# Kernel optimization log

Measured on AMD Instinct MI355X. Metric: run time of the kernel, lower is better.

The kernel has to match this reference:

```python
import jax, jax.numpy as jnp
import numpy as np

CHN = 64
C8 = CHN // 8          # 8
ANG_IN = 5
ANG_OUT = 5
BU, V, H, W = 8, ANG_IN, 64, 64


def setup_inputs() -> dict:
    key = jax.random.key(0)
    ks = jax.random.split(key, 7)
    s = 0.05
    buffer = jax.random.normal(ks[0], (BU, CHN, V, H, W), jnp.float32)
    # 1x1x1 Conv3d weights stored as [out_ch, in_ch]
    Wq = jax.random.normal(ks[1], (C8, CHN), jnp.float32) * s
    Wk = jax.random.normal(ks[2], (C8, CHN), jnp.float32) * s
    Wv = jax.random.normal(ks[3], (C8 * ANG_OUT, CHN), jnp.float32) * s
    Wc = jax.random.normal(ks[4], (C8 * ANG_OUT, CHN), jnp.float32) * s
    # out block: Conv3d(40->64, k=(1,1,7), pad (0,0,3)); Conv3d(64->64, k=(7,1,1), pad (3,0,0))
    W1 = jax.random.normal(ks[5], (CHN, C8 * ANG_IN, 1, 1, 7), jnp.float32) * s
    W2 = jax.random.normal(ks[6], (CHN, CHN, 7, 1, 1), jnp.float32) * s
    return {"buffer": buffer, "Wq": Wq, "Wk": Wk, "Wv": Wv, "Wc": Wc, "W1": W1, "W2": W2}


def _pointwise(Wo, x):
    # 1x1x1 Conv3d == channel GEMM
    return jnp.einsum('oc,bcvhw->bovhw', Wo, x)


def reference(buffer, Wq, Wk, Wv, Wc, W1, W2):
    bu, c, v, h, w = buffer.shape
    q = _pointwise(Wq, buffer)      # [bu, c8, v, h, w]
    k = _pointwise(Wk, buffer)      # [bu, c8, v, h, w]
    val = _pointwise(Wv, buffer)    # [bu, c8*ar_out, v, h, w]

    def flat(x):  # 'bu c v h w -> bu c h (v w)'
        return x.transpose(0, 1, 3, 2, 4).reshape(bu, x.shape[1], h, v * w)

    qf, kf, vf = flat(q), flat(k), flat(val)
    attn = jax.nn.softmax(jnp.einsum('bchm,bchn->bhmn', qf, kf), axis=-1)  # [bu,h,vw,vw]
    out = jnp.einsum('bhmn,bchn->bchm', attn, vf)                          # [bu,c8*ar_out,h,vw]
    out = out.reshape(bu, -1, h, v, w).transpose(0, 1, 3, 2, 4)            # [bu,c8*ar_out,v,h,w]

    out = out + _pointwise(Wc, buffer)
    # 'bu (c ar_out) v h w -> bu (c v) ar_out h w'
    c8 = out.shape[1] // ANG_OUT
    out = out.reshape(bu, c8, ANG_OUT, v, h, w).transpose(0, 1, 3, 2, 4, 5)
    out = out.reshape(bu, c8 * v, ANG_OUT, h, w)

    dn = ('NCDHW', 'OIDHW', 'NCDHW')
    out = jax.nn.relu(jax.lax.conv_general_dilated(
        out, W1, (1, 1, 1), [(0, 0), (0, 0), (3, 3)], dimension_numbers=dn))
    out = jax.nn.relu(jax.lax.conv_general_dilated(
        out, W2, (1, 1, 1), [(3, 3), (0, 0), (0, 0)], dimension_numbers=dn))
    return out  # [bu, chn, ar_out, h, w]
```

## Files before the change

### kernel.cpp

```cpp
#include <hip/hip_runtime.h>
#include <math.h>


typedef __attribute__((ext_vector_type(8))) short bf16x8;
typedef __attribute__((ext_vector_type(4))) short bf16x4;
typedef __attribute__((ext_vector_type(4))) float fp32x4;
typedef __attribute__((ext_vector_type(8))) unsigned short u16x8;

#define OFF_WPJ_US  0
#define OFF_W1P_US  12288
#define OFF_W2P_US  30720
#define OFF_QFH_US  13166592
#define OFF_KFH_US  14477312
#define OFF_VTH_US  15788032
#define OFF_ZB16_US 23652352
#define OFF_Z       29696

__device__ inline unsigned short f2b(float f) {
    unsigned u = __builtin_bit_cast(unsigned, f);
    u = (u + 0x7fffu + ((u >> 16) & 1u)) >> 16;
    return (unsigned short)u;
}

#if __has_builtin(__builtin_amdgcn_mfma_f32_16x16x16bf16_1k)
#define MFMA16(a, b, c) __builtin_amdgcn_mfma_f32_16x16x16bf16_1k(a, b, c, 0, 0, 0)
#else
static __device__ inline fp32x4 mfma16_asm(bf16x4 a, bf16x4 b, fp32x4 c) {
    asm("v_mfma_f32_16x16x16_bf16 %0, %1, %2, %0" : "+v"(c) : "v"(a), "v"(b));
    return c;
}
#define MFMA16(a, b, c) mfma16_asm(a, b, c)
#endif

__global__ void prep_weights(const float* __restrict__ Wq, const float* __restrict__ Wk,
                             const float* __restrict__ Wv, const float* __restrict__ Wc,
                             const float* __restrict__ W1, const float* __restrict__ W2,
                             float* __restrict__ ws) {
    int e = blockIdx.x * 256 + threadIdx.x;
    unsigned short* us = (unsigned short*)ws;
    if (e < 6144) {
        int mt = e >> 10, kt = (e >> 9) & 1, lane = (e >> 3) & 63, j = e & 7;
        int m = mt * 16 + (lane & 15);
        int k = kt * 32 + ((lane >> 4) & 3) * 8 + j;
        float v;
        if (m < 8)       v = Wq[m * 64 + k];
        else if (m < 16) v = Wk[(m - 8) * 64 + k];
        else if (m < 56) v = Wv[(m - 16) * 64 + k];
        else             v = Wc[(m - 56) * 64 + k];
        us[OFF_WPJ_US + e] = f2b(v);
    } else if (e < 6144 + 18432) {
        int t = e - 6144;
        int j = t & 7, lane = (t >> 3) & 63, ks = (t >> 9) % 9, wid = t / 4608;
        int oc = wid * 16 + (lane & 15);
        int k = ks * 32 + (lane >> 4) * 8 + j;
        float v = 0.f;
        if (k < 280) { int kw = k / 40, ic = k % 40; v = W1[oc * 280 + ic * 7 + kw]; }
        us[OFF_W1P_US + t] = f2b(v);
    } else if (e < 6144 + 18432 + 28672) {
        int t = e - 6144 - 18432;
        int j = t & 7, lane = (t >> 3) & 63, kk = (t >> 9) & 1, kd = (t >> 10) % 7, wid = t / 7168;
        int oc = wid * 16 + (lane & 15);
        int ic = kk * 32 + (lane >> 4) * 8 + j;
        us[OFF_W2P_US + t] = f2b(W2[oc * 448 + ic * 7 + kd]);
    }
}

__global__ __launch_bounds__(256) void proj_kernel(const float* __restrict__ buf,
                                                   float* __restrict__ ws) {
    __shared__ alignas(16) float xs[64 * 64];
    int b = blockIdx.x;
    int h = b & 63;
    int v = (b >> 6) % 5;
    int bu = b / 320;
    int tid = threadIdx.x, wid = tid >> 6, lane = tid & 63;
    int col = lane & 15, quad = lane >> 4;

    const float* xbase = buf + ((bu * 64) * 5 + v) * 4096 + h * 64;
    for (int e = tid; e < 1024; e += 256) {
        int c = e >> 4, wq = e & 15;
        *(float4*)&xs[c * 64 + wq * 4] = *(const float4*)&xbase[c * 20480 + wq * 4];
    }

    const unsigned short* wpj = (const unsigned short*)ws + OFF_WPJ_US;
    bf16x8 aw[6][2];
    #pragma unroll
    for (int mt = 0; mt < 6; mt++)
        #pragma unroll
        for (int kt = 0; kt < 2; kt++)
            aw[mt][kt] = *(const bf16x8*)&wpj[((mt * 2 + kt) * 64 + lane) * 8];

    __syncthreads();

    int n0 = wid * 16;
    bf16x8 xb[2];
    #pragma unroll
    for (int kt = 0; kt < 2; kt++) {
        u16x8 t;
        #pragma unroll
        for (int j = 0; j < 8; j++)
            t[j] = f2b(xs[(kt * 32 + quad * 8 + j) * 64 + n0 + col]);
        xb[kt] = __builtin_bit_cast(bf16x8, t);
    }

    fp32x4 acc[6];
    #pragma unroll
    for (int mt = 0; mt < 6; mt++) acc[mt] = (fp32x4){0.f, 0.f, 0.f, 0.f};
    #pragma unroll
    for (int kt = 0; kt < 2; kt++)
        #pragma unroll
        for (int mt = 0; mt < 6; mt++)
            acc[mt] = __builtin_amdgcn_mfma_f32_16x16x32_bf16(aw[mt][kt], xb[kt], acc[mt], 0, 0, 0);

    int site = bu * 64 + h;
    int w = n0 + col;
    int n_flat = v * 64 + w;
    unsigned short* base = (unsigned short*)ws;
    unsigned short* qfh = base + OFF_QFH_US;
    unsigned short* kfh = base + OFF_KFH_US;
    unsigned short* vth = base + OFF_VTH_US;
    float* z = ws + OFF_Z;

    {
        ushort4 o;
        o.x = f2b(acc[0][0]); o.y = f2b(acc[0][1]); o.z = f2b(acc[0][2]); o.w = f2b(acc[0][3]);
        if (quad < 2) *(ushort4*)&qfh[(site * 320 + n_flat) * 8 + quad * 4] = o;
        else          *(ushort4*)&kfh[(site * 320 + n_flat) * 8 + (quad - 2) * 4] = o;
    }
    #pragma unroll
    for (int r = 0; r < 4; r++) {
        vth[(site * 48 + quad * 4 + r) * 320 + n_flat]      = f2b(acc[1][r]);
        vth[(site * 48 + 16 + quad * 4 + r) * 320 + n_flat] = f2b(acc[2][r]);
    }
    if (quad < 2) {
        #pragma unroll
        for (int r = 0; r < 4; r++)
            vth[(site * 48 + 32 + quad * 4 + r) * 320 + n_flat] = f2b(acc[3][r]);
    } else {
        #pragma unroll
        for (int r = 0; r < 4; r++) {
            int jc = (quad - 2) * 4 + r;
            z[((bu * 40 + (jc / 5) * 5 + v) * 5 + (jc % 5)) * 4096 + h * 64 + w] = acc[3][r];
        }
    }
    #pragma unroll
    for (int r = 0; r < 4; r++) {
        int jc4 = 8 + quad * 4 + r;
        z[((bu * 40 + (jc4 / 5) * 5 + v) * 5 + (jc4 % 5)) * 4096 + h * 64 + w] = acc[4][r];
        int jc5 = 24 + quad * 4 + r;
        z[((bu * 40 + (jc5 / 5) * 5 + v) * 5 + (jc5 % 5)) * 4096 + h * 64 + w] = acc[5][r];
    }
    if (wid == 3) {
        #pragma unroll
        for (int j = 40; j < 48; j++)
            vth[(site * 48 + j) * 320 + v * 64 + lane] =
                (j == 40) ? (unsigned short)0x3F80 : (unsigned short)0;
    }
}

__global__ __launch_bounds__(256, 2) void attn_kernel(float* __restrict__ ws) {
    __shared__ alignas(16) short vt[48 * 328];
    __shared__ alignas(16) short kl[320 * 8];

    int bid = blockIdx.x;
    int chunk = bid >> 9;
    int site = bid & 511;
    int bu = site >> 6, h = site & 63;
    int tid = threadIdx.x;
    int wid = tid >> 6, lane = tid & 63;
    int col = lane & 15, quad = lane >> 4;

    const unsigned short* base = (const unsigned short*)ws;
    const unsigned short* qfh = base + OFF_QFH_US + site * 320 * 8;
    const unsigned short* kfh = base + OFF_KFH_US + site * 320 * 8;
    const unsigned short* vsrc = base + OFF_VTH_US + site * 48 * 320;
    float* z = ws + OFF_Z;
    unsigned short* zb16 = (unsigned short*)ws + OFF_ZB16_US;

    for (int e = tid; e < 48 * 40; e += 256) {
        int row = e / 40, c8o = e % 40;
        *(u16x8*)&vt[row * 328 + c8o * 8] = *(const u16x8*)&vsrc[row * 320 + c8o * 8];
    }
    for (int e = tid; e < 320; e += 256)
        *(u16x8*)&kl[e * 8] = *(const u16x8*)&kfh[e * 8];
    __syncthreads();

    int off0[4], off1[4], off2[4];
    #pragma unroll
    for (int r = 0; r < 4; r++) {
        int j0 = quad * 4 + r, j1 = j0 + 16, j2 = j0 + 32;
        off0[r] = ((j0 / 5) * 25 + j0 % 5) * 4096;
        off1[r] = ((j1 / 5) * 25 + j1 % 5) * 4096;
        off2[r] = ((j2 / 5) * 25 + j2 % 5) * 4096;
    }

    int mt = chunk * 4 + wid;
    int m0 = mt * 16;

    int v_idx = m0 >> 6, w0 = m0 & 63;
    int sbase = (bu * 200 + v_idx * 5) * 4096 + h * 64 + w0 + col;
    float* zb = z + sbase;
    float zold0[4], zold1[4], zold2[4];
    #pragma unroll
    for (int r = 0; r < 4; r++) {
        zold0[r] = zb[off0[r]];
        zold1[r] = zb[off1[r]];
        zold2[r] = (quad < 2) ? zb[off2[r]] : 0.f;
    }

    bf16x8 qa = (bf16x8)0;
    if (quad == 0) qa = *(const bf16x8*)&qfh[(m0 + col) * 8];

    fp32x4 acc0 = {0.f, 0.f, 0.f, 0.f}, acc1 = acc0, acc2 = acc0;

    for (int cc = 0; cc < 4; cc++) {
        fp32x4 sT[5];
        #pragma unroll
        for (int u = 0; u < 5; u++) {
            int nt = cc * 5 + u;
            bf16x8 kb = *(const bf16x8*)&kl[(nt * 16 + col) * 8];
            sT[u] = __builtin_amdgcn_mfma_f32_16x16x32_bf16(
                kb, qa, (fp32x4){0.f, 0.f, 0.f, 0.f}, 0, 0, 0);
        }
        #pragma unroll
        for (int u = 0; u < 5; u++) {
            int nt = cc * 5 + u;
            bf16x4 pa;
            #pragma unroll
            for (int r = 0; r < 4; r++) pa[r] = (short)f2b(__expf(sT[u][r]));
            const short* vb = &vt[nt * 16 + quad * 4];
            acc0 = MFMA16(*(const bf16x4*)&vb[(col) * 328],      pa, acc0);
            acc1 = MFMA16(*(const bf16x4*)&vb[(16 + col) * 328], pa, acc1);
            acc2 = MFMA16(*(const bf16x4*)&vb[(32 + col) * 328], pa, acc2);
        }
    }

    float L = __shfl(acc2[0], 32 + col, 64);
    float inv = 1.f / L;

    unsigned short* zsb = zb16 + sbase;
    #pragma unroll
    for (int r = 0; r < 4; r++) {
        zsb[off0[r]] = f2b(zold0[r] + acc0[r] * inv);
        zsb[off1[r]] = f2b(zold1[r] + acc1[r] * inv);
        if (quad < 2) zsb[off2[r]] = f2b(zold2[r] + acc2[r] * inv);
    }
}

__global__ __launch_bounds__(256) void conv12_mfma(float* __restrict__ ws,
                                                   float* __restrict__ out) {
    __shared__ alignas(16) unsigned short ol[320 * 72];
    __shared__ alignas(16) unsigned short zl2[2][72 * 40];
    int b = blockIdx.x;
    int bu = b >> 6, h = b & 63;
    int tid = threadIdx.x, wid = tid >> 6, lane = tid & 63;
    int col = lane & 15, quad = lane >> 4;
    const unsigned short* zb16 = (const unsigned short*)ws + OFF_ZB16_US;

    const unsigned short* w1p = (const unsigned short*)ws + OFF_W1P_US;
    bf16x8 a1[9];
    #pragma unroll
    for (int ks = 0; ks < 9; ks++)
        a1[ks] = *(const bf16x8*)&w1p[((wid * 9 + ks) * 64 + lane) * 8];

    #define STAGE_AR(ar_, bufi_)                                                          \
        {                                                                                 \
            unsigned short* zb_ = zl2[bufi_];                                             \
            if (tid < 160) {                                                              \
                int wpi = tid / 20, icd = tid % 20;                                       \
                int wp = wpi < 3 ? wpi : wpi + 64;                                        \
                ((unsigned*)zb_)[wp * 20 + icd] = 0u;                                     \
            }                                                                             \
            for (int icq = wid; icq < 10; icq += 4) {                                     \
                const unsigned short* src = zb16 + ((bu * 40 + icq * 4) * 5 + (ar_)) * 4096 + h * 64 + lane; \
                ushort4 v4;                                                               \
                v4.x = src[0];                                                            \
                v4.y = src[20480];                                                        \
                v4.z = src[40960];                                                        \
                v4.w = src[61440];                                                        \
                *(ushort4*)&zb_[(3 + lane) * 40 + icq * 4] = v4;                          \
            }                                                                             \
        }

    STAGE_AR(0, 0);
    __syncthreads();
    for (int ar = 0; ar < 5; ar++) {
        if (ar < 4) STAGE_AR(ar + 1, (ar + 1) & 1);
        const unsigned short* zb = zl2[ar & 1];
        #pragma unroll
        for (int w4 = 0; w4 < 4; w4++) {
            int bb = (w4 * 16 + col) * 40;
            fp32x4 acc = {0.f, 0.f, 0.f, 0.f};
            #pragma unroll
            for (int ks = 0; ks < 9; ks++) {
                bf16x8 bf = *(const bf16x8*)&zb[bb + ks * 32 + quad * 8];
                acc = __builtin_amdgcn_mfma_f32_16x16x32_bf16(a1[ks], bf, acc, 0, 0, 0);
            }
            ushort4 o;
            o.x = f2b(fmaxf(acc[0], 0.f));
            o.y = f2b(fmaxf(acc[1], 0.f));
            o.z = f2b(fmaxf(acc[2], 0.f));
            o.w = f2b(fmaxf(acc[3], 0.f));
            *(ushort4*)&ol[(ar * 64 + w4 * 16 + col) * 72 + wid * 16 + quad * 4] = o;
        }
        __syncthreads();
    }
    #undef STAGE_AR

    const unsigned short* w2p = (const unsigned short*)ws + OFF_W2P_US;
    bf16x8 a2[7][2];
    #pragma unroll
    for (int kd = 0; kd < 7; kd++)
        #pragma unroll
        for (int kk = 0; kk < 2; kk++)
            a2[kd][kk] = *(const bf16x8*)&w2p[(((wid * 7 + kd) * 2 + kk) * 64 + lane) * 8];

    for (int nt = 0; nt < 20; nt++) {
        int ar = nt >> 2, wbase = (nt & 3) * 16;
        fp32x4 acc = {0.f, 0.f, 0.f, 0.f};
        #pragma unroll
        for (int kd = 0; kd < 7; kd++) {
            int arp = ar + kd - 3;
            if (arp >= 0 && arp < 5) {
                int sb = (arp * 64 + wbase + col) * 72;
                #pragma unroll
                for (int kk = 0; kk < 2; kk++) {
                    bf16x8 bf = *(const bf16x8*)&ol[sb + kk * 32 + quad * 8];
                    acc = __builtin_amdgcn_mfma_f32_16x16x32_bf16(a2[kd][kk], bf, acc, 0, 0, 0);
                }
            }
        }
        int w = wbase + col;
        #pragma unroll
        for (int r = 0; r < 4; r++) {
            int oc = wid * 16 + quad * 4 + r;
            out[((bu * 64 + oc) * 5 + ar) * 4096 + h * 64 + w] = fmaxf(acc[r], 0.f);
        }
    }
}

extern "C" void kernel_launch(void* const* d_in, const int* in_sizes, int n_in,
                              void* d_out, int out_size, void* d_ws, size_t ws_size,
                              hipStream_t stream) {
    const float* buf = (const float*)d_in[0];
    const float* Wq  = (const float*)d_in[1];
    const float* Wk  = (const float*)d_in[2];
    const float* Wv  = (const float*)d_in[3];
    const float* Wc  = (const float*)d_in[4];
    const float* W1  = (const float*)d_in[5];
    const float* W2  = (const float*)d_in[6];
    float* ws  = (float*)d_ws;
    float* out = (float*)d_out;

    prep_weights<<<208, 256, 0, stream>>>(Wq, Wk, Wv, Wc, W1, W2, ws);
    proj_kernel<<<2560, 256, 0, stream>>>(buf, ws);
    attn_kernel<<<2560, 256, 0, stream>>>(ws);
    conv12_mfma<<<512, 256, 0, stream>>>(ws, out);
}
```

Before: 155.9 us.

## Fuse attention and conv stages into one per-site kernel with eight waves

Merges the attention kernel and the two-stage conv kernel into a single 512-thread kernel launched once per (batch, row) site. Each block stages K and V into shared memory once, runs all 20 query tiles over three rounds, then reuses the same shared memory for the conv stages. The conv work is split across twice as many waves. This removes one launch and the repeated K/V staging that happened across the five chunk blocks per site. In exchange, the grid drops from 2560 to 512 blocks, the last attention round leaves half the waves idle, and the conv reads intermediate global data written by the same block after a barrier.

```diff
diff --git a/kernel.cpp b/kernel.cpp
--- a/kernel.cpp
+++ b/kernel.cpp
@@ -157,13 +157,13 @@
     }
 }
 
-__global__ __launch_bounds__(256, 2) void attn_kernel(float* __restrict__ ws) {
-    __shared__ alignas(16) short vt[48 * 328];
-    __shared__ alignas(16) short kl[320 * 8];
-
-    int bid = blockIdx.x;
-    int chunk = bid >> 9;
-    int site = bid & 511;
+__global__ __launch_bounds__(512, 2) void attn_conv(float* __restrict__ ws,
+                                                    float* __restrict__ out) {
+    __shared__ alignas(16) unsigned char smem[57600];
+    short* vt = (short*)smem;
+    short* kl = (short*)(smem + 31488);
+
+    int site = blockIdx.x;
     int bu = site >> 6, h = site & 63;
     int tid = threadIdx.x;
     int wid = tid >> 6, lane = tid & 63;
@@ -176,11 +176,11 @@
     float* z = ws + OFF_Z;
     unsigned short* zb16 = (unsigned short*)ws + OFF_ZB16_US;
 
-    for (int e = tid; e < 48 * 40; e += 256) {
+    for (int e = tid; e < 48 * 40; e += 512) {
         int row = e / 40, c8o = e % 40;
         *(u16x8*)&vt[row * 328 + c8o * 8] = *(const u16x8*)&vsrc[row * 320 + c8o * 8];
     }
-    for (int e = tid; e < 320; e += 256)
+    for (int e = tid; e < 320; e += 512)
         *(u16x8*)&kl[e * 8] = *(const u16x8*)&kfh[e * 8];
     __syncthreads();
 
@@ -193,84 +193,81 @@
         off2[r] = ((j2 / 5) * 25 + j2 % 5) * 4096;
     }
 
-    int mt = chunk * 4 + wid;
-    int m0 = mt * 16;
-
-    int v_idx = m0 >> 6, w0 = m0 & 63;
-    int sbase = (bu * 200 + v_idx * 5) * 4096 + h * 64 + w0 + col;
-    float* zb = z + sbase;
-    float zold0[4], zold1[4], zold2[4];
-    #pragma unroll
-    for (int r = 0; r < 4; r++) {
-        zold0[r] = zb[off0[r]];
-        zold1[r] = zb[off1[r]];
-        zold2[r] = (quad < 2) ? zb[off2[r]] : 0.f;
-    }
-
-    bf16x8 qa = (bf16x8)0;
-    if (quad == 0) qa = *(const bf16x8*)&qfh[(m0 + col) * 8];
-
-    fp32x4 acc0 = {0.f, 0.f, 0.f, 0.f}, acc1 = acc0, acc2 = acc0;
-
-    for (int cc = 0; cc < 4; cc++) {
-        fp32x4 sT[5];
-        #pragma unroll
-        for (int u = 0; u < 5; u++) {
-            int nt = cc * 5 + u;
-            bf16x8 kb = *(const bf16x8*)&kl[(nt * 16 + col) * 8];
-            sT[u] = __builtin_amdgcn_mfma_f32_16x16x32_bf16(
-                kb, qa, (fp32x4){0.f, 0.f, 0.f, 0.f}, 0, 0, 0);
-        }
-        #pragma unroll
-        for (int u = 0; u < 5; u++) {
-            int nt = cc * 5 + u;
-            bf16x4 pa;
+    for (int round = 0; round < 3; round++) {
+        int mt = round * 8 + wid;
+        if (mt >= 20) break;
+        int m0 = mt * 16;
+
+        int v_idx = m0 >> 6, w0 = m0 & 63;
+        int sbase = (bu * 200 + v_idx * 5) * 4096 + h * 64 + w0 + col;
+        float* zb = z + sbase;
+        float zold0[4], zold1[4], zold2[4];
+        #pragma unroll
+        for (int r = 0; r < 4; r++) {
+            zold0[r] = zb[off0[r]];
+            zold1[r] = zb[off1[r]];
+            zold2[r] = (quad < 2) ? zb[off2[r]] : 0.f;
+        }
+
+        bf16x8 qa = (bf16x8)0;
+        if (quad == 0) qa = *(const bf16x8*)&qfh[(m0 + col) * 8];
+
+        fp32x4 acc0 = {0.f, 0.f, 0.f, 0.f}, acc1 = acc0, acc2 = acc0;
+
+        for (int cc = 0; cc < 4; cc++) {
+            fp32x4 sT[5];
             #pragma unroll
-            for (int r = 0; r < 4; r++) pa[r] = (short)f2b(__expf(sT[u][r]));
-            const short* vb = &vt[nt * 16 + quad * 4];
-            acc0 = MFMA16(*(const bf16x4*)&vb[(col) * 328],      pa, acc0);
-            acc1 = MFMA16(*(const bf16x4*)&vb[(16 + col) * 328], pa, acc1);
-            acc2 = MFMA16(*(const bf16x4*)&vb[(32 + col) * 328], pa, acc2);
-        }
-    }
-
-    float L = __shfl(acc2[0], 32 + col, 64);
-    float inv = 1.f / L;
-
-    unsigned short* zsb = zb16 + sbase;
-    #pragma unroll
-    for (int r = 0; r < 4; r++) {
-        zsb[off0[r]] = f2b(zold0[r] + acc0[r] * inv);
-        zsb[off1[r]] = f2b(zold1[r] + acc1[r] * inv);
-        if (quad < 2) zsb[off2[r]] = f2b(zold2[r] + acc2[r] * inv);
-    }
-}
-
-__global__ __launch_bounds__(256) void conv12_mfma(float* __restrict__ ws,
-                                                   float* __restrict__ out) {
-    __shared__ alignas(16) unsigned short ol[320 * 72];
-    __shared__ alignas(16) unsigned short zl2[2][72 * 40];
-    int b = blockIdx.x;
-    int bu = b >> 6, h = b & 63;
-    int tid = threadIdx.x, wid = tid >> 6, lane = tid & 63;
-    int col = lane & 15, quad = lane >> 4;
-    const unsigned short* zb16 = (const unsigned short*)ws + OFF_ZB16_US;
+            for (int u = 0; u < 5; u++) {
+                int nt = cc * 5 + u;
+                bf16x8 kb = *(const bf16x8*)&kl[(nt * 16 + col) * 8];
+                sT[u] = __builtin_amdgcn_mfma_f32_16x16x32_bf16(
+                    kb, qa, (fp32x4){0.f, 0.f, 0.f, 0.f}, 0, 0, 0);
+            }
+            #pragma unroll
+            for (int u = 0; u < 5; u++) {
+                int nt = cc * 5 + u;
+                bf16x4 pa;
+                #pragma unroll
+                for (int r = 0; r < 4; r++) pa[r] = (short)f2b(__expf(sT[u][r]));
+                const short* vb = &vt[nt * 16 + quad * 4];
+                acc0 = MFMA16(*(const bf16x4*)&vb[(col) * 328],      pa, acc0);
+                acc1 = MFMA16(*(const bf16x4*)&vb[(16 + col) * 328], pa, acc1);
+                acc2 = MFMA16(*(const bf16x4*)&vb[(32 + col) * 328], pa, acc2);
+            }
+        }
+
+        float L = __shfl(acc2[0], 32 + col, 64);
+        float inv = 1.f / L;
+
+        unsigned short* zsb = zb16 + sbase;
+        #pragma unroll
+        for (int r = 0; r < 4; r++) {
+            zsb[off0[r]] = f2b(zold0[r] + acc0[r] * inv);
+            zsb[off1[r]] = f2b(zold1[r] + acc1[r] * inv);
+            if (quad < 2) zsb[off2[r]] = f2b(zold2[r] + acc2[r] * inv);
+        }
+    }
+    __syncthreads();
+
+    unsigned short* ol = (unsigned short*)smem;
+    unsigned short* zl2 = (unsigned short*)(smem + 46080);
+    int g = wid & 3, half = wid >> 2;
 
     const unsigned short* w1p = (const unsigned short*)ws + OFF_W1P_US;
     bf16x8 a1[9];
     #pragma unroll
     for (int ks = 0; ks < 9; ks++)
-        a1[ks] = *(const bf16x8*)&w1p[((wid * 9 + ks) * 64 + lane) * 8];
+        a1[ks] = *(const bf16x8*)&w1p[((g * 9 + ks) * 64 + lane) * 8];
 
     #define STAGE_AR(ar_, bufi_)                                                          \
         {                                                                                 \
-            unsigned short* zb_ = zl2[bufi_];                                             \
+            unsigned short* zb_ = zl2 + (bufi_) * 2880;                                   \
             if (tid < 160) {                                                              \
                 int wpi = tid / 20, icd = tid % 20;                                       \
                 int wp = wpi < 3 ? wpi : wpi + 64;                                        \
                 ((unsigned*)zb_)[wp * 20 + icd] = 0u;                                     \
             }                                                                             \
-            for (int icq = wid; icq < 10; icq += 4) {                                     \
+            for (int icq = wid; icq < 10; icq += 8) {                                     \
                 const unsigned short* src = zb16 + ((bu * 40 + icq * 4) * 5 + (ar_)) * 4096 + h * 64 + lane; \
                 ushort4 v4;                                                               \
                 v4.x = src[0];                                                            \
@@ -285,14 +282,15 @@
     __syncthreads();
     for (int ar = 0; ar < 5; ar++) {
         if (ar < 4) STAGE_AR(ar + 1, (ar + 1) & 1);
-        const unsigned short* zb = zl2[ar & 1];
-        #pragma unroll
-        for (int w4 = 0; w4 < 4; w4++) {
+        const unsigned short* zbl = zl2 + (ar & 1) * 2880;
+        #pragma unroll
+        for (int w4h = 0; w4h < 2; w4h++) {
+            int w4 = half * 2 + w4h;
             int bb = (w4 * 16 + col) * 40;
             fp32x4 acc = {0.f, 0.f, 0.f, 0.f};
             #pragma unroll
             for (int ks = 0; ks < 9; ks++) {
-                bf16x8 bf = *(const bf16x8*)&zb[bb + ks * 32 + quad * 8];
+                bf16x8 bf = *(const bf16x8*)&zbl[bb + ks * 32 + quad * 8];
                 acc = __builtin_amdgcn_mfma_f32_16x16x32_bf16(a1[ks], bf, acc, 0, 0, 0);
             }
             ushort4 o;
@@ -300,7 +298,7 @@
             o.y = f2b(fmaxf(acc[1], 0.f));
             o.z = f2b(fmaxf(acc[2], 0.f));
             o.w = f2b(fmaxf(acc[3], 0.f));
-            *(ushort4*)&ol[(ar * 64 + w4 * 16 + col) * 72 + wid * 16 + quad * 4] = o;
+            *(ushort4*)&ol[(ar * 64 + w4 * 16 + col) * 72 + g * 16 + quad * 4] = o;
         }
         __syncthreads();
     }
@@ -312,9 +310,10 @@
     for (int kd = 0; kd < 7; kd++)
         #pragma unroll
         for (int kk = 0; kk < 2; kk++)
-            a2[kd][kk] = *(const bf16x8*)&w2p[(((wid * 7 + kd) * 2 + kk) * 64 + lane) * 8];
-
-    for (int nt = 0; nt < 20; nt++) {
+            a2[kd][kk] = *(const bf16x8*)&w2p[(((g * 7 + kd) * 2 + kk) * 64 + lane) * 8];
+
+    for (int i = 0; i < 10; i++) {
+        int nt = half * 10 + i;
         int ar = nt >> 2, wbase = (nt & 3) * 16;
         fp32x4 acc = {0.f, 0.f, 0.f, 0.f};
         #pragma unroll
@@ -332,7 +331,7 @@
         int w = wbase + col;
         #pragma unroll
         for (int r = 0; r < 4; r++) {
-            int oc = wid * 16 + quad * 4 + r;
+            int oc = g * 16 + quad * 4 + r;
             out[((bu * 64 + oc) * 5 + ar) * 4096 + h * 64 + w] = fmaxf(acc[r], 0.f);
         }
     }
@@ -353,6 +352,5 @@
 
     prep_weights<<<208, 256, 0, stream>>>(Wq, Wk, Wv, Wc, W1, W2, ws);
     proj_kernel<<<2560, 256, 0, stream>>>(buf, ws);
-    attn_kernel<<<2560, 256, 0, stream>>>(ws);
-    conv12_mfma<<<512, 256, 0, stream>>>(ws, out);
-}
+    attn_conv<<<512, 512, 0, stream>>>(ws, out);
+}
```

After: 143.4 us. 1.09x faster.
